# Performance work log

Hardware: AMD Instinct MI355X
Metric: run time of the kernel (lower is better)

Reference implementation:

```python
import jax, jax.numpy as jnp
import numpy as np

# ---- problem constants (mirror AdjustInstanceArea __init__ args) ----
NUM_NODES = 2_000_000
NUM_MOVABLE = 1_500_000
NUM_FILLER = 400_000
NUM_NETS = 1_500_000
PINS_PER_NET = 4                       # uniform netpin_start = arange(0, P+1, 4)
NUM_PINS = NUM_NETS * PINS_PER_NET
XL, XH, YL, YH = 0.0, 1000.0, 0.0, 1000.0
NBX = NBY = 512
BIN_W = (XH - XL) / NBX
BIN_H = (YH - YL) / NBY
UNIT_H_CAP = 1.5                       # unit horizontal routing capacity
UNIT_V_CAP = 1.5                       # unit vertical routing capacity
MAX_RATE = 2.0                         # max_route_opt_adjust_rate
MIN_RATE = 1.0 / MAX_RATE
EPS = 1e-6


def setup_inputs() -> dict:
    key = jax.random.key(0)
    k = jax.random.split(key, 4)
    x = jax.random.uniform(k[0], (NUM_NODES,), jnp.float32, XL, XH - 4.0)
    y = jax.random.uniform(k[1], (NUM_NODES,), jnp.float32, YL, YH - 4.0)
    pos = jnp.concatenate([x, y])                      # [2*num_nodes], x then y

    # pins clustered around net centers (realistic small net bboxes)
    rng = np.random.default_rng(0)
    centers = rng.uniform(0.0, 1000.0, size=(NUM_NETS, 1, 2)).astype(np.float32)
    jit = rng.uniform(-20.0, 20.0, size=(NUM_NETS, PINS_PER_NET, 2)).astype(np.float32)
    ppos = np.clip(centers + jit, 0.0, 1000.0)         # [nets, pins_per_net, 2], in net order

    # flat_netpin: pin ids grouped by net; pin_pos indexed by pin id
    flat_netpin = rng.permutation(NUM_PINS).astype(np.int32)
    px = np.empty(NUM_PINS, np.float32); py = np.empty(NUM_PINS, np.float32)
    px[flat_netpin] = ppos[..., 0].reshape(-1)
    py[flat_netpin] = ppos[..., 1].reshape(-1)
    pin_pos = jnp.concatenate([jnp.asarray(px), jnp.asarray(py)])  # [2*num_pins]

    pin2net = jnp.asarray(np.repeat(np.arange(NUM_NETS, dtype=np.int32), PINS_PER_NET))

    node_size_x = jax.random.uniform(k[2], (NUM_NODES,), jnp.float32, 1.0, 4.0)
    node_size_y = jax.random.uniform(k[3], (NUM_NODES,), jnp.float32, 1.0, 4.0)
    return {"pos": pos, "pin_pos": pin_pos,
            "node_size_x": node_size_x, "node_size_y": node_size_y,
            "flat_netpin": jnp.asarray(flat_netpin), "pin2net": pin2net}


def _rect_accum(vals, blx, bly, bhx, bhy):
    """Accumulate vals over inclusive bin rectangles via difference map + 2D cumsum."""
    D = jnp.zeros((NBX + 1, NBY + 1), vals.dtype)
    D = D.at[blx, bly].add(vals)
    D = D.at[bhx + 1, bly].add(-vals)
    D = D.at[blx, bhy + 1].add(-vals)
    D = D.at[bhx + 1, bhy + 1].add(vals)
    return jnp.cumsum(jnp.cumsum(D, axis=0), axis=1)[:NBX, :NBY]


def reference(pos, pin_pos, node_size_x, node_size_y, flat_netpin, pin2net):
    # ---- InstanceRouteOptimizationArea: RUDY routing demand per bin ----
    px = pin_pos[:NUM_PINS][flat_netpin].reshape(NUM_NETS, PINS_PER_NET)
    py = pin_pos[NUM_PINS:][flat_netpin].reshape(NUM_NETS, PINS_PER_NET)
    net_xl = jnp.min(px, axis=1); net_xh = jnp.max(px, axis=1)
    net_yl = jnp.min(py, axis=1); net_yh = jnp.max(py, axis=1)
    bw = net_xh - net_xl
    bh = net_yh - net_yl
    barea = jnp.maximum(bw * bh, EPS)
    dens_h = bw / barea                                # horizontal wire density
    dens_v = bh / barea                                # vertical wire density

    blx = jnp.clip(jnp.floor((net_xl - XL) / BIN_W), 0, NBX - 1).astype(jnp.int32)
    bhx = jnp.clip(jnp.floor((net_xh - XL) / BIN_W), 0, NBX - 1).astype(jnp.int32)
    bly = jnp.clip(jnp.floor((net_yl - YL) / BIN_H), 0, NBY - 1).astype(jnp.int32)
    bhy = jnp.clip(jnp.floor((net_yh - YL) / BIN_H), 0, NBY - 1).astype(jnp.int32)

    util_h = _rect_accum(dens_h, blx, bly, bhx, bhy) / UNIT_H_CAP
    util_v = _rect_accum(dens_v, blx, bly, bhx, bhy) / UNIT_V_CAP

    # per-movable-node utilization (gather at node center bin)
    x = pos[:NUM_NODES]; y = pos[NUM_NODES:]
    nsx_m = node_size_x[:NUM_MOVABLE]; nsy_m = node_size_y[:NUM_MOVABLE]
    cx = x[:NUM_MOVABLE] + 0.5 * nsx_m
    cy = y[:NUM_MOVABLE] + 0.5 * nsy_m
    bix = jnp.clip(jnp.floor((cx - XL) / BIN_W), 0, NBX - 1).astype(jnp.int32)
    biy = jnp.clip(jnp.floor((cy - YL) / BIN_H), 0, NBY - 1).astype(jnp.int32)
    util = jnp.maximum(util_h[bix, biy], util_v[bix, biy])
    ratio = jnp.clip(util, MIN_RATE, MAX_RATE)

    area_old = nsx_m * nsy_m
    instance_route_area = area_old * ratio

    # ---- AdjustInstanceArea: rescale under max_total_area budget ----
    filler_area_old = jnp.sum(node_size_x[NUM_NODES - NUM_FILLER:] *
                              node_size_y[NUM_NODES - NUM_FILLER:])
    max_total_area = jnp.sum(area_old) + filler_area_old
    scale = jnp.minimum(1.0, max_total_area / jnp.maximum(jnp.sum(instance_route_area), EPS))
    new_area = instance_route_area * scale
    sr = jnp.sqrt(new_area / jnp.maximum(area_old, EPS))
    nsx_new = nsx_m * sr
    nsy_new = nsy_m * sr

    # keep cell centers fixed while resizing
    x_out = x.at[:NUM_MOVABLE].add(0.5 * (nsx_m - nsx_new))
    y_out = y.at[:NUM_MOVABLE].add(0.5 * (nsy_m - nsy_new))

    # fillers absorb leftover area budget
    fscale = jnp.sqrt(jnp.maximum(max_total_area - jnp.sum(new_area), 0.0) /
                      jnp.maximum(filler_area_old, EPS))
    nsx_out = node_size_x.at[:NUM_MOVABLE].set(nsx_new)
    nsx_out = nsx_out.at[NUM_NODES - NUM_FILLER:].multiply(fscale)
    nsy_out = node_size_y.at[:NUM_MOVABLE].set(nsy_new)
    nsy_out = nsy_out.at[NUM_NODES - NUM_FILLER:].multiply(fscale)

    return jnp.concatenate([x_out, y_out, nsx_out, nsy_out])  # [4*num_nodes]
```

## Files before the change

### kernel.cpp

```cpp
#include <hip/hip_runtime.h>
#include <math.h>

#define N_NODES   2000000
#define N_MOVABLE 1500000
#define N_FILLER  400000
#define N_NETS    1500000
#define N_PINS    (N_NETS * 4)
#define NB        512
#define NT        16
#define TILE      32
#define NBUCKET   (NT * NT)
#define CAP       10240
#define NMAPS     8
#define RED_BLOCKS 512
#define NPB       2048

__device__ __forceinline__ int bin_idx(float v) {
    float b = floorf(v / 1.953125f);
    b = fminf(fmaxf(b, 0.0f), 511.0f);
    return (int)b;
}

__global__ void pack_kernel(const float* __restrict__ pin_pos,
                            float2* __restrict__ pp) {
    int i = blockIdx.x * blockDim.x + threadIdx.x;
    if (i >= N_PINS / 4) return;
    float4 a = reinterpret_cast<const float4*>(pin_pos)[i];
    float4 b = reinterpret_cast<const float4*>(pin_pos + N_PINS)[i];
    float4* o = reinterpret_cast<float4*>(pp + 4 * (size_t)i);
    o[0] = make_float4(a.x, b.x, a.y, b.y);
    o[1] = make_float4(a.z, b.z, a.w, b.w);
}

template <bool PACKED>
__device__ __forceinline__ float4 make_rec(const float* __restrict__ pin_pos,
                                           const float2* __restrict__ pp,
                                           int4 fp, int* bucket) {
    float2 p0, p1, p2, p3;
    if (PACKED) {
        p0 = pp[fp.x]; p1 = pp[fp.y]; p2 = pp[fp.z]; p3 = pp[fp.w];
    } else {
        p0 = make_float2(pin_pos[fp.x], pin_pos[N_PINS + fp.x]);
        p1 = make_float2(pin_pos[fp.y], pin_pos[N_PINS + fp.y]);
        p2 = make_float2(pin_pos[fp.z], pin_pos[N_PINS + fp.z]);
        p3 = make_float2(pin_pos[fp.w], pin_pos[N_PINS + fp.w]);
    }
    float xl = fminf(fminf(p0.x, p1.x), fminf(p2.x, p3.x));
    float xh = fmaxf(fmaxf(p0.x, p1.x), fmaxf(p2.x, p3.x));
    float yl = fminf(fminf(p0.y, p1.y), fminf(p2.y, p3.y));
    float yh = fmaxf(fmaxf(p0.y, p1.y), fmaxf(p2.y, p3.y));
    float bw = xh - xl, bh = yh - yl;
    float barea = fmaxf(bw * bh, 1e-6f);
    float vh = (bw / barea) * (1.0f / 1.5f);
    float vv = (bh / barea) * (1.0f / 1.5f);
    unsigned blx = bin_idx(xl), bhx = bin_idx(xh);
    unsigned bly = bin_idx(yl), bhy = bin_idx(yh);
    *bucket = (int)((bly >> 5) * NT + (blx >> 5));
    float4 r;
    r.x = vh; r.y = vv;
    r.z = __uint_as_float(blx | (bly << 16));
    r.w = __uint_as_float((bhx + 1) | ((bhy + 1) << 16));
    return r;
}

template <bool PACKED>
__global__ __launch_bounds__(1024)
void gather_bin_kernel(const float* __restrict__ pin_pos,
                       const float2* __restrict__ pp,
                       const int*  __restrict__ fnp,
                       float4* __restrict__ slab,
                       unsigned* __restrict__ g_ptr) {
    __shared__ unsigned hist[NBUCKET];
    __shared__ unsigned base[NBUCKET];
    int t = threadIdx.x;
    if (t < NBUCKET) hist[t] = 0;
    __syncthreads();

    int n0 = blockIdx.x * NPB + t;
    int n1 = n0 + 1024;
    bool v0 = (n0 < N_NETS), v1 = (n1 < N_NETS);

    int4 fpA = v0 ? *reinterpret_cast<const int4*>(fnp + 4 * (size_t)n0) : make_int4(0,0,0,0);
    int4 fpB = v1 ? *reinterpret_cast<const int4*>(fnp + 4 * (size_t)n1) : make_int4(0,0,0,0);

    float4 r0, r1; int b0 = 0, b1 = 0; unsigned rk0 = 0, rk1 = 0;
    if (v0) { r0 = make_rec<PACKED>(pin_pos, pp, fpA, &b0); rk0 = atomicAdd(&hist[b0], 1u); }
    if (v1) { r1 = make_rec<PACKED>(pin_pos, pp, fpB, &b1); rk1 = atomicAdd(&hist[b1], 1u); }
    __syncthreads();
    if (t < NBUCKET) {
        unsigned c = hist[t];
        base[t] = c ? atomicAdd(&g_ptr[t], c) : 0u;
    }
    __syncthreads();
    if (v0) { unsigned s = base[b0] + rk0; if (s < CAP) slab[(size_t)b0 * CAP + s] = r0; }
    if (v1) { unsigned s = base[b1] + rk1; if (s < CAP) slab[(size_t)b1 * CAP + s] = r1; }
}

__global__ __launch_bounds__(256)
void accum_kernel(const float4* __restrict__ slab,
                  const unsigned* __restrict__ g_cnt,
                  float2* __restrict__ Dp) {
    __shared__ float2 acc[64 * 64];
    int wg = blockIdx.x;
    int h = wg & 1, tile = wg >> 1;
    int tx = tile & (NT - 1), ty = tile >> 4;

    for (int i = threadIdx.x; i < 64 * 64; i += 256) acc[i] = make_float2(0.f, 0.f);
    __syncthreads();

    int x0 = tx * TILE, y0 = ty * TILE;
    unsigned cnt = min(g_cnt[tile], (unsigned)CAP);
    unsigned lo = h ? cnt / 2 : 0u;
    unsigned hi = h ? cnt : cnt / 2;
    const float4* recs = slab + (size_t)tile * CAP;

    for (unsigned i = lo + threadIdx.x; i < hi; i += 256) {
        float4 r = recs[i];
        unsigned zlo = __float_as_uint(r.z), zhi = __float_as_uint(r.w);
        int ax0 = (int)(zlo & 0xffffu), ay0 = (int)(zlo >> 16);
        int ax1 = (int)(zhi & 0xffffu), ay1 = (int)(zhi >> 16);
        int X0 = ax0 - x0, Y0 = ay0 - y0;
        int X1 = ax1 - x0, Y1 = ay1 - y0;
        bool okx1 = (ax1 < NB), oky1 = (ay1 < NB);
        atomicAdd(&acc[X0 * 64 + Y0].x,  r.x);
        atomicAdd(&acc[X0 * 64 + Y0].y,  r.y);
        if (okx1) { atomicAdd(&acc[X1 * 64 + Y0].x, -r.x); atomicAdd(&acc[X1 * 64 + Y0].y, -r.y); }
        if (oky1) { atomicAdd(&acc[X0 * 64 + Y1].x, -r.x); atomicAdd(&acc[X0 * 64 + Y1].y, -r.y); }
        if (okx1 && oky1) { atomicAdd(&acc[X1 * 64 + Y1].x, r.x); atomicAdd(&acc[X1 * 64 + Y1].y, r.y); }
    }
    __syncthreads();

    int m = h * 4 + (ty & 1) * 2 + (tx & 1);
    float2* D = Dp + (size_t)m * NB * NB;
    for (int i = threadIdx.x; i < 64 * 64; i += 256) {
        int X = i >> 6, Y = i & 63;
        int gx = x0 + X, gy = y0 + Y;
        if (gx < NB && gy < NB) D[(size_t)gx * NB + gy] = acc[i];
    }
}

__global__ void scanA_kernel(const float2* __restrict__ Dp,
                             float2* __restrict__ S) {
    __shared__ float2 s[NB];
    int x = blockIdx.x, t = threadIdx.x;
    float2 a = make_float2(0.f, 0.f);
    #pragma unroll
    for (int m = 0; m < NMAPS; ++m) {
        if (((m & 1) && x < TILE) || ((m & 2) && t < TILE)) continue;
        float2 v = Dp[(size_t)m * NB * NB + (size_t)x * NB + t];
        a.x += v.x; a.y += v.y;
    }
    s[t] = a;
    __syncthreads();
    for (int off = 1; off < NB; off <<= 1) {
        float2 u = s[t];
        if (t >= off) { float2 w = s[t - off]; u.x += w.x; u.y += w.y; }
        __syncthreads();
        s[t] = u;
        __syncthreads();
    }
    S[(size_t)x * NB + t] = s[t];
}

__global__ void scanB_kernel(float2* __restrict__ S) {
    __shared__ float2 s[NB];
    int y = blockIdx.x, t = threadIdx.x;
    s[t] = S[(size_t)t * NB + y];
    __syncthreads();
    for (int off = 1; off < NB; off <<= 1) {
        float2 u = s[t];
        if (t >= off) { float2 w = s[t - off]; u.x += w.x; u.y += w.y; }
        __syncthreads();
        s[t] = u;
        __syncthreads();
    }
    S[(size_t)t * NB + y] = s[t];
}

__global__ __launch_bounds__(256)
void reduce_kernel(const float* __restrict__ pos,
                   const float* __restrict__ nsx,
                   const float* __restrict__ nsy,
                   const float2* __restrict__ S,
                   double* __restrict__ partials) {
    const int MQ = N_MOVABLE / 4;
    const int TQ = MQ + N_FILLER / 4;
    double a_old = 0.0, a_route = 0.0, a_fill = 0.0;
    int stride = gridDim.x * blockDim.x;
    for (int q = blockIdx.x * blockDim.x + threadIdx.x; q < TQ; q += stride) {
        if (q < MQ) {
            int i = 4 * q;
            float4 x4  = *reinterpret_cast<const float4*>(pos + i);
            float4 y4  = *reinterpret_cast<const float4*>(pos + N_NODES + i);
            float4 sx4 = *reinterpret_cast<const float4*>(nsx + i);
            float4 sy4 = *reinterpret_cast<const float4*>(nsy + i);
            float xs[4] = {x4.x, x4.y, x4.z, x4.w};
            float ys[4] = {y4.x, y4.y, y4.z, y4.w};
            float sxs[4] = {sx4.x, sx4.y, sx4.z, sx4.w};
            float sys[4] = {sy4.x, sy4.y, sy4.z, sy4.w};
            #pragma unroll
            for (int k = 0; k < 4; ++k) {
                int bx = bin_idx(xs[k] + 0.5f * sxs[k]);
                int by = bin_idx(ys[k] + 0.5f * sys[k]);
                float2 u2 = S[(size_t)bx * NB + by];
                float ratio = fminf(fmaxf(fmaxf(u2.x, u2.y), 0.5f), 2.0f);
                float area = sxs[k] * sys[k];
                a_old += (double)area;
                a_route += (double)(area * ratio);
            }
        } else {
            int j = (N_NODES - N_FILLER) + 4 * (q - MQ);
            float4 sx4 = *reinterpret_cast<const float4*>(nsx + j);
            float4 sy4 = *reinterpret_cast<const float4*>(nsy + j);
            a_fill += (double)(sx4.x * sy4.x + sx4.y * sy4.y +
                               sx4.z * sy4.z + sx4.w * sy4.w);
        }
    }
    for (int off = 32; off > 0; off >>= 1) {
        a_old   += __shfl_down(a_old, off);
        a_route += __shfl_down(a_route, off);
        a_fill  += __shfl_down(a_fill, off);
    }
    __shared__ double sd[4][3];
    int wid = threadIdx.x >> 6, lane = threadIdx.x & 63;
    if (lane == 0) { sd[wid][0] = a_old; sd[wid][1] = a_route; sd[wid][2] = a_fill; }
    __syncthreads();
    if (threadIdx.x == 0) {
        double s0 = 0, s1 = 0, s2 = 0;
        for (int w = 0; w < 4; ++w) { s0 += sd[w][0]; s1 += sd[w][1]; s2 += sd[w][2]; }
        partials[blockIdx.x * 3 + 0] = s0;
        partials[blockIdx.x * 3 + 1] = s1;
        partials[blockIdx.x * 3 + 2] = s2;
    }
}

__global__ void finish_kernel(const double* __restrict__ partials,
                              double* __restrict__ sums) {
    int t = threadIdx.x;
    double s0 = partials[t * 3 + 0];
    double s1 = partials[t * 3 + 1];
    double s2 = partials[t * 3 + 2];
    for (int off = 32; off > 0; off >>= 1) {
        s0 += __shfl_down(s0, off);
        s1 += __shfl_down(s1, off);
        s2 += __shfl_down(s2, off);
    }
    __shared__ double sd[8][3];
    int wid = t >> 6, lane = t & 63;
    if (lane == 0) { sd[wid][0] = s0; sd[wid][1] = s1; sd[wid][2] = s2; }
    __syncthreads();
    if (t == 0) {
        double a = 0, b = 0, c = 0;
        for (int w = 0; w < 8; ++w) { a += sd[w][0]; b += sd[w][1]; c += sd[w][2]; }
        sums[0] = a; sums[1] = b; sums[2] = c;
    }
}

__global__ __launch_bounds__(256)
void final_kernel(const float* __restrict__ pos,
                  const float* __restrict__ nsx,
                  const float* __restrict__ nsy,
                  const float2* __restrict__ S,
                  const double* __restrict__ sums,
                  float* __restrict__ out) {
    double sum_area  = sums[0];
    double sum_route = sums[1];
    double fill_old  = sums[2];
    double max_total = sum_area + fill_old;

    float scale = fminf(1.0f, (float)(max_total / fmax(sum_route, 1e-6)));
    float sum_new = (float)(scale * (float)sum_route);
    float fscale = sqrtf(fmaxf((float)max_total - sum_new, 0.0f) /
                         fmaxf((float)fill_old, 1e-6f));

    int q = blockIdx.x * blockDim.x + threadIdx.x;
    if (q >= N_NODES / 4) return;
    int i = 4 * q;

    float4 x4  = *reinterpret_cast<const float4*>(pos + i);
    float4 y4  = *reinterpret_cast<const float4*>(pos + N_NODES + i);
    float4 sx4 = *reinterpret_cast<const float4*>(nsx + i);
    float4 sy4 = *reinterpret_cast<const float4*>(nsy + i);

    float xs[4] = {x4.x, x4.y, x4.z, x4.w};
    float ys[4] = {y4.x, y4.y, y4.z, y4.w};
    float sxs[4] = {sx4.x, sx4.y, sx4.z, sx4.w};
    float sys[4] = {sy4.x, sy4.y, sy4.z, sy4.w};

    if (i < N_MOVABLE) {
        #pragma unroll
        for (int k = 0; k < 4; ++k) {
            int bx = bin_idx(xs[k] + 0.5f * sxs[k]);
            int by = bin_idx(ys[k] + 0.5f * sys[k]);
            float2 u2 = S[(size_t)bx * NB + by];
            float ratio = fminf(fmaxf(fmaxf(u2.x, u2.y), 0.5f), 2.0f);
            float area = sxs[k] * sys[k];
            float new_area = area * ratio * scale;
            float sr = sqrtf(new_area / fmaxf(area, 1e-6f));
            float sx_new = sxs[k] * sr, sy_new = sys[k] * sr;
            xs[k] = xs[k] + 0.5f * (sxs[k] - sx_new);
            ys[k] = ys[k] + 0.5f * (sys[k] - sy_new);
            sxs[k] = sx_new; sys[k] = sy_new;
        }
    } else if (i >= N_NODES - N_FILLER) {
        #pragma unroll
        for (int k = 0; k < 4; ++k) { sxs[k] *= fscale; sys[k] *= fscale; }
    }

    *reinterpret_cast<float4*>(out + i)               = make_float4(xs[0], xs[1], xs[2], xs[3]);
    *reinterpret_cast<float4*>(out + N_NODES + i)     = make_float4(ys[0], ys[1], ys[2], ys[3]);
    *reinterpret_cast<float4*>(out + 2 * N_NODES + i) = make_float4(sxs[0], sxs[1], sxs[2], sxs[3]);
    *reinterpret_cast<float4*>(out + 3 * N_NODES + i) = make_float4(sys[0], sys[1], sys[2], sys[3]);
}

extern "C" void kernel_launch(void* const* d_in, const int* in_sizes, int n_in,
                              void* d_out, int out_size, void* d_ws, size_t ws_size,
                              hipStream_t stream) {
    const float* pos         = (const float*)d_in[0];
    const float* pin_pos     = (const float*)d_in[1];
    const float* nsx         = (const float*)d_in[2];
    const float* nsy         = (const float*)d_in[3];
    const int*   flat_netpin = (const int*)d_in[4];
    float* out = (float*)d_out;

    const size_t pp_b   = (size_t)N_PINS * sizeof(float2);
    const size_t slab_b = (size_t)NBUCKET * CAP * sizeof(float4);
    const size_t dp_b   = (size_t)NMAPS * NB * NB * sizeof(float2);
    const size_t s_b    = (size_t)NB * NB * sizeof(float2);
    const size_t part_b = (size_t)RED_BLOCKS * 3 * sizeof(double);
    const size_t gp_b   = 4096;

    const size_t need_primary = pp_b + slab_b + gp_b + 64;

    float2* pp = nullptr;
    float4* slab; float2* Dp; float2* S; double* partials;
    unsigned* g_ptr; double* sums;
    char* base = (char*)d_ws;
    bool packed = (ws_size >= need_primary);
    if (packed) {
        pp       = (float2*)base;
        Dp       = (float2*)base;
        S        = (float2*)(base + dp_b);
        partials = (double*)(base + dp_b + s_b);
        slab     = (float4*)(base + pp_b);
        g_ptr    = (unsigned*)(base + pp_b + slab_b);
        sums     = (double*)(base + pp_b + slab_b + gp_b);
    } else {
        slab     = (float4*)base;
        Dp       = (float2*)(base + slab_b);
        S        = (float2*)(base + slab_b + dp_b);
        partials = (double*)(base + slab_b + dp_b + s_b);
        g_ptr    = (unsigned*)(base + slab_b + dp_b + s_b + part_b);
        sums     = (double*)((char*)g_ptr + gp_b);
    }

    hipMemsetAsync(g_ptr, 0, NBUCKET * sizeof(unsigned), stream);

    const int GB_BLOCKS = (N_NETS + NPB - 1) / NPB;
    if (packed) {
        pack_kernel<<<(N_PINS / 4 + 255) / 256, 256, 0, stream>>>(pin_pos, pp);
        gather_bin_kernel<true><<<GB_BLOCKS, 1024, 0, stream>>>(pin_pos, pp, flat_netpin, slab, g_ptr);
    } else {
        gather_bin_kernel<false><<<GB_BLOCKS, 1024, 0, stream>>>(pin_pos, nullptr, flat_netpin, slab, g_ptr);
    }

    accum_kernel<<<2 * NBUCKET, 256, 0, stream>>>(slab, g_ptr, Dp);
    scanA_kernel<<<NB, NB, 0, stream>>>(Dp, S);
    scanB_kernel<<<NB, NB, 0, stream>>>(S);

    reduce_kernel<<<RED_BLOCKS, 256, 0, stream>>>(pos, nsx, nsy, S, partials);
    finish_kernel<<<1, 512, 0, stream>>>(partials, sums);
    final_kernel<<<(N_NODES / 4 + 255) / 256, 256, 0, stream>>>(pos, nsx, nsy, S, sums, out);
}
```

Before: 267.9 us.

## Fuse post-binning stages into one cooperative persistent kernel with grid syncs

Replaces the accum, two scan, reduce, finish and final launches with one cooperative mega-kernel of 1024 blocks that separates the stages with grid-wide syncs, and keeps the separate launches as a fallback. Accumulation is split four ways per tile (16 partial maps), gather handles four nets per thread, scans use 256 threads with two elements each, and the g_ptr memset moves into pack_kernel. The goal is to remove launch gaps and tail effects between small stages. In exchange it adds grid-sync cost, requires co-residency of 1024 blocks with 32KB LDS each, and doubles the size of the partial-map buffer.

Result: slower. 797.5 us (+197.7%).

```diff
diff --git a/kernel.cpp b/kernel.cpp
--- a/kernel.cpp
+++ b/kernel.cpp
@@ -1,4 +1,5 @@
 #include <hip/hip_runtime.h>
+#include <hip/hip_cooperative_groups.h>
 #include <math.h>
 
 #define N_NODES   2000000
@@ -11,9 +12,12 @@
 #define TILE      32
 #define NBUCKET   (NT * NT)
 #define CAP       10240
-#define NMAPS     8
-#define RED_BLOCKS 512
-#define NPB       2048
+#define NMAPS     16
+#define NPB       4096
+#define MEGA_BLOCKS 1024
+#define GSZ       (MEGA_BLOCKS * 256)
+
+namespace cg = cooperative_groups;
 
 __device__ __forceinline__ int bin_idx(float v) {
     float b = floorf(v / 1.953125f);
@@ -22,7 +26,9 @@
 }
 
 __global__ void pack_kernel(const float* __restrict__ pin_pos,
-                            float2* __restrict__ pp) {
+                            float2* __restrict__ pp,
+                            unsigned* __restrict__ g_ptr) {
+    if (blockIdx.x == 0 && threadIdx.x < NBUCKET) g_ptr[threadIdx.x] = 0u;
     int i = blockIdx.x * blockDim.x + threadIdx.x;
     if (i >= N_PINS / 4) return;
     float4 a = reinterpret_cast<const float4*>(pin_pos)[i];
@@ -77,44 +83,56 @@
     __syncthreads();
 
     int n0 = blockIdx.x * NPB + t;
-    int n1 = n0 + 1024;
-    bool v0 = (n0 < N_NETS), v1 = (n1 < N_NETS);
-
-    int4 fpA = v0 ? *reinterpret_cast<const int4*>(fnp + 4 * (size_t)n0) : make_int4(0,0,0,0);
-    int4 fpB = v1 ? *reinterpret_cast<const int4*>(fnp + 4 * (size_t)n1) : make_int4(0,0,0,0);
-
-    float4 r0, r1; int b0 = 0, b1 = 0; unsigned rk0 = 0, rk1 = 0;
-    if (v0) { r0 = make_rec<PACKED>(pin_pos, pp, fpA, &b0); rk0 = atomicAdd(&hist[b0], 1u); }
-    if (v1) { r1 = make_rec<PACKED>(pin_pos, pp, fpB, &b1); rk1 = atomicAdd(&hist[b1], 1u); }
+    bool v[4]; int4 fp[4]; float4 r[4]; int b[4]; unsigned rk[4];
+    #pragma unroll
+    for (int k = 0; k < 4; ++k) {
+        int n = n0 + k * 1024;
+        v[k] = (n < N_NETS);
+        fp[k] = v[k] ? *reinterpret_cast<const int4*>(fnp + 4 * (size_t)n)
+                     : make_int4(0, 0, 0, 0);
+    }
+    #pragma unroll
+    for (int k = 0; k < 4; ++k) {
+        b[k] = 0;
+        if (v[k]) r[k] = make_rec<PACKED>(pin_pos, pp, fp[k], &b[k]);
+    }
+    #pragma unroll
+    for (int k = 0; k < 4; ++k) {
+        rk[k] = v[k] ? atomicAdd(&hist[b[k]], 1u) : 0u;
+    }
     __syncthreads();
     if (t < NBUCKET) {
         unsigned c = hist[t];
         base[t] = c ? atomicAdd(&g_ptr[t], c) : 0u;
     }
     __syncthreads();
-    if (v0) { unsigned s = base[b0] + rk0; if (s < CAP) slab[(size_t)b0 * CAP + s] = r0; }
-    if (v1) { unsigned s = base[b1] + rk1; if (s < CAP) slab[(size_t)b1 * CAP + s] = r1; }
-}
-
-__global__ __launch_bounds__(256)
-void accum_kernel(const float4* __restrict__ slab,
-                  const unsigned* __restrict__ g_cnt,
-                  float2* __restrict__ Dp) {
-    __shared__ float2 acc[64 * 64];
-    int wg = blockIdx.x;
-    int h = wg & 1, tile = wg >> 1;
+    #pragma unroll
+    for (int k = 0; k < 4; ++k) {
+        if (v[k]) {
+            unsigned s = base[b[k]] + rk[k];
+            if (s < CAP) slab[(size_t)b[k] * CAP + s] = r[k];
+        }
+    }
+}
+
+
+__device__ __forceinline__ void stage_accum(const float4* __restrict__ slab,
+                                            const unsigned* __restrict__ g_cnt,
+                                            float2* __restrict__ Dp,
+                                            float2* acc, int wg, int tid) {
+    int h = wg & 3, tile = wg >> 2;
     int tx = tile & (NT - 1), ty = tile >> 4;
 
-    for (int i = threadIdx.x; i < 64 * 64; i += 256) acc[i] = make_float2(0.f, 0.f);
+    for (int i = tid; i < 64 * 64; i += 256) acc[i] = make_float2(0.f, 0.f);
     __syncthreads();
 
     int x0 = tx * TILE, y0 = ty * TILE;
     unsigned cnt = min(g_cnt[tile], (unsigned)CAP);
-    unsigned lo = h ? cnt / 2 : 0u;
-    unsigned hi = h ? cnt : cnt / 2;
+    unsigned lo = (cnt * (unsigned)h) >> 2;
+    unsigned hi = (cnt * (unsigned)(h + 1)) >> 2;
     const float4* recs = slab + (size_t)tile * CAP;
 
-    for (unsigned i = lo + threadIdx.x; i < hi; i += 256) {
+    for (unsigned i = lo + tid; i < hi; i += 256) {
         float4 r = recs[i];
         unsigned zlo = __float_as_uint(r.z), zhi = __float_as_uint(r.w);
         int ax0 = (int)(zlo & 0xffffu), ay0 = (int)(zlo >> 16);
@@ -132,62 +150,72 @@
 
     int m = h * 4 + (ty & 1) * 2 + (tx & 1);
     float2* D = Dp + (size_t)m * NB * NB;
-    for (int i = threadIdx.x; i < 64 * 64; i += 256) {
+    for (int i = tid; i < 64 * 64; i += 256) {
         int X = i >> 6, Y = i & 63;
         int gx = x0 + X, gy = y0 + Y;
         if (gx < NB && gy < NB) D[(size_t)gx * NB + gy] = acc[i];
     }
 }
 
-__global__ void scanA_kernel(const float2* __restrict__ Dp,
-                             float2* __restrict__ S) {
-    __shared__ float2 s[NB];
-    int x = blockIdx.x, t = threadIdx.x;
-    float2 a = make_float2(0.f, 0.f);
+__device__ __forceinline__ void stage_scanA(const float2* __restrict__ Dp,
+                                            float2* __restrict__ S,
+                                            float2* s, int x, int tid) {
     #pragma unroll
-    for (int m = 0; m < NMAPS; ++m) {
-        if (((m & 1) && x < TILE) || ((m & 2) && t < TILE)) continue;
-        float2 v = Dp[(size_t)m * NB * NB + (size_t)x * NB + t];
-        a.x += v.x; a.y += v.y;
-    }
-    s[t] = a;
+    for (int k = 0; k < 2; ++k) {
+        int y = tid + k * 256;
+        float2 a = make_float2(0.f, 0.f);
+        #pragma unroll
+        for (int m = 0; m < NMAPS; ++m) {
+            if (((m & 1) && x < TILE) || ((m & 2) && y < TILE)) continue;
+            float2 v = Dp[(size_t)m * NB * NB + (size_t)x * NB + y];
+            a.x += v.x; a.y += v.y;
+        }
+        s[y] = a;
+    }
     __syncthreads();
     for (int off = 1; off < NB; off <<= 1) {
-        float2 u = s[t];
-        if (t >= off) { float2 w = s[t - off]; u.x += w.x; u.y += w.y; }
+        float2 u0 = s[tid], u1 = s[tid + 256];
+        float2 w0 = (tid >= off) ? s[tid - off] : make_float2(0.f, 0.f);
+        float2 w1 = s[tid + 256 - off];
         __syncthreads();
-        s[t] = u;
+        if (tid >= off) { u0.x += w0.x; u0.y += w0.y; }
+        u1.x += w1.x; u1.y += w1.y;
+        s[tid] = u0; s[tid + 256] = u1;
         __syncthreads();
     }
-    S[(size_t)x * NB + t] = s[t];
-}
-
-__global__ void scanB_kernel(float2* __restrict__ S) {
-    __shared__ float2 s[NB];
-    int y = blockIdx.x, t = threadIdx.x;
-    s[t] = S[(size_t)t * NB + y];
+    S[(size_t)x * NB + tid] = s[tid];
+    S[(size_t)x * NB + tid + 256] = s[tid + 256];
+}
+
+__device__ __forceinline__ void stage_scanB(float2* __restrict__ S,
+                                            float2* s, int y, int tid) {
+    s[tid] = S[(size_t)tid * NB + y];
+    s[tid + 256] = S[(size_t)(tid + 256) * NB + y];
     __syncthreads();
     for (int off = 1; off < NB; off <<= 1) {
-        float2 u = s[t];
-        if (t >= off) { float2 w = s[t - off]; u.x += w.x; u.y += w.y; }
+        float2 u0 = s[tid], u1 = s[tid + 256];
+        float2 w0 = (tid >= off) ? s[tid - off] : make_float2(0.f, 0.f);
+        float2 w1 = s[tid + 256 - off];
         __syncthreads();
-        s[t] = u;
+        if (tid >= off) { u0.x += w0.x; u0.y += w0.y; }
+        u1.x += w1.x; u1.y += w1.y;
+        s[tid] = u0; s[tid + 256] = u1;
         __syncthreads();
     }
-    S[(size_t)t * NB + y] = s[t];
-}
-
-__global__ __launch_bounds__(256)
-void reduce_kernel(const float* __restrict__ pos,
-                   const float* __restrict__ nsx,
-                   const float* __restrict__ nsy,
-                   const float2* __restrict__ S,
-                   double* __restrict__ partials) {
+    S[(size_t)tid * NB + y] = s[tid];
+    S[(size_t)(tid + 256) * NB + y] = s[tid + 256];
+}
+
+__device__ __forceinline__ void stage_reduce(const float* __restrict__ pos,
+                                             const float* __restrict__ nsx,
+                                             const float* __restrict__ nsy,
+                                             const float2* __restrict__ S,
+                                             double* __restrict__ partials,
+                                             float2* smem, int bid, int tid) {
     const int MQ = N_MOVABLE / 4;
     const int TQ = MQ + N_FILLER / 4;
     double a_old = 0.0, a_route = 0.0, a_fill = 0.0;
-    int stride = gridDim.x * blockDim.x;
-    for (int q = blockIdx.x * blockDim.x + threadIdx.x; q < TQ; q += stride) {
+    for (int q = bid * 256 + tid; q < TQ; q += GSZ) {
         if (q < MQ) {
             int i = 4 * q;
             float4 x4  = *reinterpret_cast<const float4*>(pos + i);
@@ -221,96 +249,159 @@
         a_route += __shfl_down(a_route, off);
         a_fill  += __shfl_down(a_fill, off);
     }
-    __shared__ double sd[4][3];
-    int wid = threadIdx.x >> 6, lane = threadIdx.x & 63;
-    if (lane == 0) { sd[wid][0] = a_old; sd[wid][1] = a_route; sd[wid][2] = a_fill; }
-    __syncthreads();
-    if (threadIdx.x == 0) {
+    double* sd = (double*)smem;
+    int wid = tid >> 6, lane = tid & 63;
+    if (lane == 0) { sd[wid * 3 + 0] = a_old; sd[wid * 3 + 1] = a_route; sd[wid * 3 + 2] = a_fill; }
+    __syncthreads();
+    if (tid == 0) {
         double s0 = 0, s1 = 0, s2 = 0;
-        for (int w = 0; w < 4; ++w) { s0 += sd[w][0]; s1 += sd[w][1]; s2 += sd[w][2]; }
-        partials[blockIdx.x * 3 + 0] = s0;
-        partials[blockIdx.x * 3 + 1] = s1;
-        partials[blockIdx.x * 3 + 2] = s2;
-    }
-}
-
-__global__ void finish_kernel(const double* __restrict__ partials,
-                              double* __restrict__ sums) {
-    int t = threadIdx.x;
-    double s0 = partials[t * 3 + 0];
-    double s1 = partials[t * 3 + 1];
-    double s2 = partials[t * 3 + 2];
+        for (int w = 0; w < 4; ++w) { s0 += sd[w * 3]; s1 += sd[w * 3 + 1]; s2 += sd[w * 3 + 2]; }
+        partials[bid * 3 + 0] = s0;
+        partials[bid * 3 + 1] = s1;
+        partials[bid * 3 + 2] = s2;
+    }
+}
+
+__device__ __forceinline__ void stage_finish(const double* __restrict__ partials,
+                                             double* __restrict__ sums,
+                                             float2* smem, int tid) {
+    double s0 = 0, s1 = 0, s2 = 0;
+    for (int r = tid; r < MEGA_BLOCKS; r += 256) {
+        s0 += partials[r * 3 + 0];
+        s1 += partials[r * 3 + 1];
+        s2 += partials[r * 3 + 2];
+    }
     for (int off = 32; off > 0; off >>= 1) {
         s0 += __shfl_down(s0, off);
         s1 += __shfl_down(s1, off);
         s2 += __shfl_down(s2, off);
     }
-    __shared__ double sd[8][3];
-    int wid = t >> 6, lane = t & 63;
-    if (lane == 0) { sd[wid][0] = s0; sd[wid][1] = s1; sd[wid][2] = s2; }
-    __syncthreads();
-    if (t == 0) {
+    double* sd = (double*)smem;
+    int wid = tid >> 6, lane = tid & 63;
+    if (lane == 0) { sd[wid * 3 + 0] = s0; sd[wid * 3 + 1] = s1; sd[wid * 3 + 2] = s2; }
+    __syncthreads();
+    if (tid == 0) {
         double a = 0, b = 0, c = 0;
-        for (int w = 0; w < 8; ++w) { a += sd[w][0]; b += sd[w][1]; c += sd[w][2]; }
+        for (int w = 0; w < 4; ++w) { a += sd[w * 3]; b += sd[w * 3 + 1]; c += sd[w * 3 + 2]; }
         sums[0] = a; sums[1] = b; sums[2] = c;
     }
 }
 
-__global__ __launch_bounds__(256)
-void final_kernel(const float* __restrict__ pos,
-                  const float* __restrict__ nsx,
-                  const float* __restrict__ nsy,
-                  const float2* __restrict__ S,
-                  const double* __restrict__ sums,
-                  float* __restrict__ out) {
+__device__ __forceinline__ void stage_final(const float* __restrict__ pos,
+                                            const float* __restrict__ nsx,
+                                            const float* __restrict__ nsy,
+                                            const float2* __restrict__ S,
+                                            const double* __restrict__ sums,
+                                            float* __restrict__ out,
+                                            int bid, int tid) {
     double sum_area  = sums[0];
     double sum_route = sums[1];
     double fill_old  = sums[2];
     double max_total = sum_area + fill_old;
-
     float scale = fminf(1.0f, (float)(max_total / fmax(sum_route, 1e-6)));
     float sum_new = (float)(scale * (float)sum_route);
     float fscale = sqrtf(fmaxf((float)max_total - sum_new, 0.0f) /
                          fmaxf((float)fill_old, 1e-6f));
 
-    int q = blockIdx.x * blockDim.x + threadIdx.x;
-    if (q >= N_NODES / 4) return;
-    int i = 4 * q;
-
-    float4 x4  = *reinterpret_cast<const float4*>(pos + i);
-    float4 y4  = *reinterpret_cast<const float4*>(pos + N_NODES + i);
-    float4 sx4 = *reinterpret_cast<const float4*>(nsx + i);
-    float4 sy4 = *reinterpret_cast<const float4*>(nsy + i);
-
-    float xs[4] = {x4.x, x4.y, x4.z, x4.w};
-    float ys[4] = {y4.x, y4.y, y4.z, y4.w};
-    float sxs[4] = {sx4.x, sx4.y, sx4.z, sx4.w};
-    float sys[4] = {sy4.x, sy4.y, sy4.z, sy4.w};
-
-    if (i < N_MOVABLE) {
-        #pragma unroll
-        for (int k = 0; k < 4; ++k) {
-            int bx = bin_idx(xs[k] + 0.5f * sxs[k]);
-            int by = bin_idx(ys[k] + 0.5f * sys[k]);
-            float2 u2 = S[(size_t)bx * NB + by];
-            float ratio = fminf(fmaxf(fmaxf(u2.x, u2.y), 0.5f), 2.0f);
-            float area = sxs[k] * sys[k];
-            float new_area = area * ratio * scale;
-            float sr = sqrtf(new_area / fmaxf(area, 1e-6f));
-            float sx_new = sxs[k] * sr, sy_new = sys[k] * sr;
-            xs[k] = xs[k] + 0.5f * (sxs[k] - sx_new);
-            ys[k] = ys[k] + 0.5f * (sys[k] - sy_new);
-            sxs[k] = sx_new; sys[k] = sy_new;
+    for (int q = bid * 256 + tid; q < N_NODES / 4; q += GSZ) {
+        int i = 4 * q;
+        float4 x4  = *reinterpret_cast<const float4*>(pos + i);
+        float4 y4  = *reinterpret_cast<const float4*>(pos + N_NODES + i);
+        float4 sx4 = *reinterpret_cast<const float4*>(nsx + i);
+        float4 sy4 = *reinterpret_cast<const float4*>(nsy + i);
+        float xs[4] = {x4.x, x4.y, x4.z, x4.w};
+        float ys[4] = {y4.x, y4.y, y4.z, y4.w};
+        float sxs[4] = {sx4.x, sx4.y, sx4.z, sx4.w};
+        float sys[4] = {sy4.x, sy4.y, sy4.z, sy4.w};
+
+        if (i < N_MOVABLE) {
+            #pragma unroll
+            for (int k = 0; k < 4; ++k) {
+                int bx = bin_idx(xs[k] + 0.5f * sxs[k]);
+                int by = bin_idx(ys[k] + 0.5f * sys[k]);
+                float2 u2 = S[(size_t)bx * NB + by];
+                float ratio = fminf(fmaxf(fmaxf(u2.x, u2.y), 0.5f), 2.0f);
+                float area = sxs[k] * sys[k];
+                float new_area = area * ratio * scale;
+                float sr = sqrtf(new_area / fmaxf(area, 1e-6f));
+                float sx_new = sxs[k] * sr, sy_new = sys[k] * sr;
+                xs[k] = xs[k] + 0.5f * (sxs[k] - sx_new);
+                ys[k] = ys[k] + 0.5f * (sys[k] - sy_new);
+                sxs[k] = sx_new; sys[k] = sy_new;
+            }
+        } else if (i >= N_NODES - N_FILLER) {
+            #pragma unroll
+            for (int k = 0; k < 4; ++k) { sxs[k] *= fscale; sys[k] *= fscale; }
         }
-    } else if (i >= N_NODES - N_FILLER) {
-        #pragma unroll
-        for (int k = 0; k < 4; ++k) { sxs[k] *= fscale; sys[k] *= fscale; }
-    }
-
-    *reinterpret_cast<float4*>(out + i)               = make_float4(xs[0], xs[1], xs[2], xs[3]);
-    *reinterpret_cast<float4*>(out + N_NODES + i)     = make_float4(ys[0], ys[1], ys[2], ys[3]);
-    *reinterpret_cast<float4*>(out + 2 * N_NODES + i) = make_float4(sxs[0], sxs[1], sxs[2], sxs[3]);
-    *reinterpret_cast<float4*>(out + 3 * N_NODES + i) = make_float4(sys[0], sys[1], sys[2], sys[3]);
+
+        *reinterpret_cast<float4*>(out + i)               = make_float4(xs[0], xs[1], xs[2], xs[3]);
+        *reinterpret_cast<float4*>(out + N_NODES + i)     = make_float4(ys[0], ys[1], ys[2], ys[3]);
+        *reinterpret_cast<float4*>(out + 2 * N_NODES + i) = make_float4(sxs[0], sxs[1], sxs[2], sxs[3]);
+        *reinterpret_cast<float4*>(out + 3 * N_NODES + i) = make_float4(sys[0], sys[1], sys[2], sys[3]);
+    }
+}
+
+__global__ __launch_bounds__(256)
+void mega_kernel(const float4* __restrict__ slab,
+                 const unsigned* __restrict__ g_cnt,
+                 float2* __restrict__ Dp,
+                 float2* __restrict__ S,
+                 const float* __restrict__ pos,
+                 const float* __restrict__ nsx,
+                 const float* __restrict__ nsy,
+                 double* __restrict__ partials,
+                 double* __restrict__ sums,
+                 float* __restrict__ out) {
+    __shared__ float2 smem[4096];
+    cg::grid_group g = cg::this_grid();
+    int bid = blockIdx.x, tid = threadIdx.x;
+
+    stage_accum(slab, g_cnt, Dp, smem, bid, tid);
+    g.sync();
+    if (bid < NB) stage_scanA(Dp, S, smem, bid, tid);
+    g.sync();
+    if (bid < NB) stage_scanB(S, smem, bid, tid);
+    g.sync();
+    stage_reduce(pos, nsx, nsy, S, partials, smem, bid, tid);
+    g.sync();
+    if (bid == 0) stage_finish(partials, sums, smem, tid);
+    g.sync();
+    stage_final(pos, nsx, nsy, S, sums, out, bid, tid);
+}
+
+__global__ __launch_bounds__(256)
+void accum_kernel(const float4* __restrict__ slab, const unsigned* __restrict__ g_cnt,
+                  float2* __restrict__ Dp) {
+    __shared__ float2 smem[4096];
+    stage_accum(slab, g_cnt, Dp, smem, blockIdx.x, threadIdx.x);
+}
+__global__ __launch_bounds__(256)
+void scanA_kernel(const float2* __restrict__ Dp, float2* __restrict__ S) {
+    __shared__ float2 s[NB];
+    stage_scanA(Dp, S, s, blockIdx.x, threadIdx.x);
+}
+__global__ __launch_bounds__(256)
+void scanB_kernel(float2* __restrict__ S) {
+    __shared__ float2 s[NB];
+    stage_scanB(S, s, blockIdx.x, threadIdx.x);
+}
+__global__ __launch_bounds__(256)
+void reduce_kernel(const float* __restrict__ pos, const float* __restrict__ nsx,
+                   const float* __restrict__ nsy, const float2* __restrict__ S,
+                   double* __restrict__ partials) {
+    __shared__ float2 smem[64];
+    stage_reduce(pos, nsx, nsy, S, partials, smem, blockIdx.x, threadIdx.x);
+}
+__global__ __launch_bounds__(256)
+void finish_kernel(const double* __restrict__ partials, double* __restrict__ sums) {
+    __shared__ float2 smem[64];
+    stage_finish(partials, sums, smem, threadIdx.x);
+}
+__global__ __launch_bounds__(256)
+void final_kernel(const float* __restrict__ pos, const float* __restrict__ nsx,
+                  const float* __restrict__ nsy, const float2* __restrict__ S,
+                  const double* __restrict__ sums, float* __restrict__ out) {
+    stage_final(pos, nsx, nsy, S, sums, out, blockIdx.x, threadIdx.x);
 }
 
 extern "C" void kernel_launch(void* const* d_in, const int* in_sizes, int n_in,
@@ -327,48 +418,60 @@
     const size_t slab_b = (size_t)NBUCKET * CAP * sizeof(float4);
     const size_t dp_b   = (size_t)NMAPS * NB * NB * sizeof(float2);
     const size_t s_b    = (size_t)NB * NB * sizeof(float2);
-    const size_t part_b = (size_t)RED_BLOCKS * 3 * sizeof(double);
+    const size_t part_b = (size_t)MEGA_BLOCKS * 3 * sizeof(double);
     const size_t gp_b   = 4096;
 
-    const size_t need_primary = pp_b + slab_b + gp_b + 64;
-
-    float2* pp = nullptr;
-    float4* slab; float2* Dp; float2* S; double* partials;
-    unsigned* g_ptr; double* sums;
+    const size_t need_primary = pp_b + slab_b + gp_b + 256;
+
     char* base = (char*)d_ws;
     bool packed = (ws_size >= need_primary);
+
+    float2* pp; float4* slab; float2* Dp; float2* S;
+    double* partials; double* sums; unsigned* g_ptr;
     if (packed) {
         pp       = (float2*)base;
         Dp       = (float2*)base;
         S        = (float2*)(base + dp_b);
         partials = (double*)(base + dp_b + s_b);
+        sums     = (double*)(base + dp_b + s_b + part_b);
         slab     = (float4*)(base + pp_b);
         g_ptr    = (unsigned*)(base + pp_b + slab_b);
-        sums     = (double*)(base + pp_b + slab_b + gp_b);
     } else {
+        pp       = nullptr;
         slab     = (float4*)base;
         Dp       = (float2*)(base + slab_b);
         S        = (float2*)(base + slab_b + dp_b);
         partials = (double*)(base + slab_b + dp_b + s_b);
-        g_ptr    = (unsigned*)(base + slab_b + dp_b + s_b + part_b);
-        sums     = (double*)((char*)g_ptr + gp_b);
-    }
-
-    hipMemsetAsync(g_ptr, 0, NBUCKET * sizeof(unsigned), stream);
+        sums     = (double*)(base + slab_b + dp_b + s_b + part_b);
+        g_ptr    = (unsigned*)(base + slab_b + dp_b + s_b + part_b + 64);
+    }
 
     const int GB_BLOCKS = (N_NETS + NPB - 1) / NPB;
     if (packed) {
-        pack_kernel<<<(N_PINS / 4 + 255) / 256, 256, 0, stream>>>(pin_pos, pp);
+        pack_kernel<<<(N_PINS / 4 + 255) / 256, 256, 0, stream>>>(pin_pos, pp, g_ptr);
         gather_bin_kernel<true><<<GB_BLOCKS, 1024, 0, stream>>>(pin_pos, pp, flat_netpin, slab, g_ptr);
     } else {
+        hipMemsetAsync(g_ptr, 0, NBUCKET * sizeof(unsigned), stream);
         gather_bin_kernel<false><<<GB_BLOCKS, 1024, 0, stream>>>(pin_pos, nullptr, flat_netpin, slab, g_ptr);
     }
 
-    accum_kernel<<<2 * NBUCKET, 256, 0, stream>>>(slab, g_ptr, Dp);
-    scanA_kernel<<<NB, NB, 0, stream>>>(Dp, S);
-    scanB_kernel<<<NB, NB, 0, stream>>>(S);
-
-    reduce_kernel<<<RED_BLOCKS, 256, 0, stream>>>(pos, nsx, nsy, S, partials);
-    finish_kernel<<<1, 512, 0, stream>>>(partials, sums);
-    final_kernel<<<(N_NODES / 4 + 255) / 256, 256, 0, stream>>>(pos, nsx, nsy, S, sums, out);
-}
+    const float4* slab_c = slab;
+    const unsigned* gc = g_ptr;
+    const float* pos_c = pos; const float* nsx_c = nsx; const float* nsy_c = nsy;
+    float* out_l = out;
+    void* args[] = { (void*)&slab_c, (void*)&gc, (void*)&Dp, (void*)&S,
+                     (void*)&pos_c, (void*)&nsx_c, (void*)&nsy_c,
+                     (void*)&partials, (void*)&sums, (void*)&out_l };
+    hipError_t e = hipLaunchCooperativeKernel((void*)mega_kernel,
+                                              dim3(MEGA_BLOCKS), dim3(256),
+                                              args, 0, stream);
+    if (e != hipSuccess) {
+        (void)hipGetLastError();
+        accum_kernel <<<MEGA_BLOCKS, 256, 0, stream>>>(slab, g_ptr, Dp);
+        scanA_kernel <<<NB, 256, 0, stream>>>(Dp, S);
+        scanB_kernel <<<NB, 256, 0, stream>>>(S);
+        reduce_kernel<<<MEGA_BLOCKS, 256, 0, stream>>>(pos, nsx, nsy, S, partials);
+        finish_kernel<<<1, 256, 0, stream>>>(partials, sums);
+        final_kernel <<<MEGA_BLOCKS, 256, 0, stream>>>(pos, nsx, nsy, S, sums, out);
+    }
+}
```

## Switch accumulation to owner-tile gather with 4 slices, fewer maps, fused memset

Applied to the files above, without the earlier changes.

The accumulation kernel now has each 32x32 output tile pull records from its own bucket and the left, up and up-left neighbor buckets, split into four slices. It writes only its own tile instead of a 64x64 overlapping halo into parity-indexed maps, so the D maps drop from 8 to 4 and scanA stops skipping per-parity regions. The gather kernel processes 4 nets per thread, the g_ptr memset is folded into pack_kernel, and the reduce block count doubles with a strided finish loop. The aim is less shared memory per block, fewer global map writes and reads, and one less launch. The cost is that each accum block now reads up to four buckets' records and filters out most of them.

Result: faster. 242.1 us (-9.6%).

```diff
diff --git a/kernel.cpp b/kernel.cpp
--- a/kernel.cpp
+++ b/kernel.cpp
@@ -11,9 +11,10 @@
 #define TILE      32
 #define NBUCKET   (NT * NT)
 #define CAP       10240
-#define NMAPS     8
-#define RED_BLOCKS 512
-#define NPB       2048
+#define NSLICE    4
+#define NMAPS     NSLICE
+#define NPB       4096
+#define RED_BLOCKS 1024
 
 __device__ __forceinline__ int bin_idx(float v) {
     float b = floorf(v / 1.953125f);
@@ -22,7 +23,9 @@
 }
 
 __global__ void pack_kernel(const float* __restrict__ pin_pos,
-                            float2* __restrict__ pp) {
+                            float2* __restrict__ pp,
+                            unsigned* __restrict__ g_ptr) {
+    if (blockIdx.x == 0 && threadIdx.x < NBUCKET) g_ptr[threadIdx.x] = 0u;
     int i = blockIdx.x * blockDim.x + threadIdx.x;
     if (i >= N_PINS / 4) return;
     float4 a = reinterpret_cast<const float4*>(pin_pos)[i];
@@ -77,76 +80,108 @@
     __syncthreads();
 
     int n0 = blockIdx.x * NPB + t;
-    int n1 = n0 + 1024;
-    bool v0 = (n0 < N_NETS), v1 = (n1 < N_NETS);
-
-    int4 fpA = v0 ? *reinterpret_cast<const int4*>(fnp + 4 * (size_t)n0) : make_int4(0,0,0,0);
-    int4 fpB = v1 ? *reinterpret_cast<const int4*>(fnp + 4 * (size_t)n1) : make_int4(0,0,0,0);
-
-    float4 r0, r1; int b0 = 0, b1 = 0; unsigned rk0 = 0, rk1 = 0;
-    if (v0) { r0 = make_rec<PACKED>(pin_pos, pp, fpA, &b0); rk0 = atomicAdd(&hist[b0], 1u); }
-    if (v1) { r1 = make_rec<PACKED>(pin_pos, pp, fpB, &b1); rk1 = atomicAdd(&hist[b1], 1u); }
+    bool v[4]; int4 fp[4]; float4 r[4]; int b[4]; unsigned rk[4];
+    #pragma unroll
+    for (int k = 0; k < 4; ++k) {
+        int n = n0 + k * 1024;
+        v[k] = (n < N_NETS);
+        fp[k] = v[k] ? *reinterpret_cast<const int4*>(fnp + 4 * (size_t)n)
+                     : make_int4(0, 0, 0, 0);
+    }
+    #pragma unroll
+    for (int k = 0; k < 4; ++k) {
+        b[k] = 0;
+        if (v[k]) r[k] = make_rec<PACKED>(pin_pos, pp, fp[k], &b[k]);
+    }
+    #pragma unroll
+    for (int k = 0; k < 4; ++k) {
+        rk[k] = v[k] ? atomicAdd(&hist[b[k]], 1u) : 0u;
+    }
     __syncthreads();
     if (t < NBUCKET) {
         unsigned c = hist[t];
         base[t] = c ? atomicAdd(&g_ptr[t], c) : 0u;
     }
     __syncthreads();
-    if (v0) { unsigned s = base[b0] + rk0; if (s < CAP) slab[(size_t)b0 * CAP + s] = r0; }
-    if (v1) { unsigned s = base[b1] + rk1; if (s < CAP) slab[(size_t)b1 * CAP + s] = r1; }
+    #pragma unroll
+    for (int k = 0; k < 4; ++k) {
+        if (v[k]) {
+            unsigned s = base[b[k]] + rk[k];
+            if (s < CAP) slab[(size_t)b[k] * CAP + s] = r[k];
+        }
+    }
+}
+
+__device__ __forceinline__ void rec_process(float4 r, int x0, int y0,
+                                            float2* acc) {
+    unsigned zlo = __float_as_uint(r.z), zhi = __float_as_uint(r.w);
+    int ax0 = (int)(zlo & 0xffffu), ay0 = (int)(zlo >> 16);
+    int ax1 = (int)(zhi & 0xffffu), ay1 = (int)(zhi >> 16);
+    int X0 = ax0 - x0, Y0 = ay0 - y0;
+    int X1 = ax1 - x0, Y1 = ay1 - y0;
+    bool iX0 = (unsigned)X0 < TILE, iX1 = (unsigned)X1 < TILE;
+    bool iY0 = (unsigned)Y0 < TILE, iY1 = (unsigned)Y1 < TILE;
+    if (iX0 && iY0) { atomicAdd(&acc[X0 * TILE + Y0].x,  r.x); atomicAdd(&acc[X0 * TILE + Y0].y,  r.y); }
+    if (iX1 && iY0) { atomicAdd(&acc[X1 * TILE + Y0].x, -r.x); atomicAdd(&acc[X1 * TILE + Y0].y, -r.y); }
+    if (iX0 && iY1) { atomicAdd(&acc[X0 * TILE + Y1].x, -r.x); atomicAdd(&acc[X0 * TILE + Y1].y, -r.y); }
+    if (iX1 && iY1) { atomicAdd(&acc[X1 * TILE + Y1].x,  r.x); atomicAdd(&acc[X1 * TILE + Y1].y,  r.y); }
 }
 
 __global__ __launch_bounds__(256)
 void accum_kernel(const float4* __restrict__ slab,
                   const unsigned* __restrict__ g_cnt,
                   float2* __restrict__ Dp) {
-    __shared__ float2 acc[64 * 64];
+    __shared__ float2 acc[TILE * TILE];
     int wg = blockIdx.x;
-    int h = wg & 1, tile = wg >> 1;
+    int sl = wg & (NSLICE - 1), tile = wg >> 2;
     int tx = tile & (NT - 1), ty = tile >> 4;
-
-    for (int i = threadIdx.x; i < 64 * 64; i += 256) acc[i] = make_float2(0.f, 0.f);
+    int tid = threadIdx.x;
+
+    for (int i = tid; i < TILE * TILE; i += 256) acc[i] = make_float2(0.f, 0.f);
     __syncthreads();
 
     int x0 = tx * TILE, y0 = ty * TILE;
-    unsigned cnt = min(g_cnt[tile], (unsigned)CAP);
-    unsigned lo = h ? cnt / 2 : 0u;
-    unsigned hi = h ? cnt : cnt / 2;
-    const float4* recs = slab + (size_t)tile * CAP;
-
-    for (unsigned i = lo + threadIdx.x; i < hi; i += 256) {
-        float4 r = recs[i];
-        unsigned zlo = __float_as_uint(r.z), zhi = __float_as_uint(r.w);
-        int ax0 = (int)(zlo & 0xffffu), ay0 = (int)(zlo >> 16);
-        int ax1 = (int)(zhi & 0xffffu), ay1 = (int)(zhi >> 16);
-        int X0 = ax0 - x0, Y0 = ay0 - y0;
-        int X1 = ax1 - x0, Y1 = ay1 - y0;
-        bool okx1 = (ax1 < NB), oky1 = (ay1 < NB);
-        atomicAdd(&acc[X0 * 64 + Y0].x,  r.x);
-        atomicAdd(&acc[X0 * 64 + Y0].y,  r.y);
-        if (okx1) { atomicAdd(&acc[X1 * 64 + Y0].x, -r.x); atomicAdd(&acc[X1 * 64 + Y0].y, -r.y); }
-        if (oky1) { atomicAdd(&acc[X0 * 64 + Y1].x, -r.x); atomicAdd(&acc[X0 * 64 + Y1].y, -r.y); }
-        if (okx1 && oky1) { atomicAdd(&acc[X1 * 64 + Y1].x, r.x); atomicAdd(&acc[X1 * 64 + Y1].y, r.y); }
-    }
-    __syncthreads();
-
-    int m = h * 4 + (ty & 1) * 2 + (tx & 1);
-    float2* D = Dp + (size_t)m * NB * NB;
-    for (int i = threadIdx.x; i < 64 * 64; i += 256) {
-        int X = i >> 6, Y = i & 63;
-        int gx = x0 + X, gy = y0 + Y;
-        if (gx < NB && gy < NB) D[(size_t)gx * NB + gy] = acc[i];
-    }
-}
-
-__global__ void scanA_kernel(const float2* __restrict__ Dp,
-                             float2* __restrict__ S) {
+    #pragma unroll
+    for (int dy = -1; dy <= 0; ++dy) {
+        int sy = ty + dy; if (sy < 0) continue;
+        #pragma unroll
+        for (int dx = -1; dx <= 0; ++dx) {
+            int sx = tx + dx; if (sx < 0) continue;
+            int sb = sy * NT + sx;
+            unsigned cnt = min(g_cnt[sb], (unsigned)CAP);
+            unsigned lo = (cnt * (unsigned)sl) >> 2;
+            unsigned hi = (cnt * (unsigned)(sl + 1)) >> 2;
+            const float4* recs = slab + (size_t)sb * CAP;
+            unsigned i = lo + tid;
+            for (; i + 768 < hi; i += 1024) {
+                float4 r0 = recs[i];
+                float4 r1 = recs[i + 256];
+                float4 r2 = recs[i + 512];
+                float4 r3 = recs[i + 768];
+                rec_process(r0, x0, y0, acc);
+                rec_process(r1, x0, y0, acc);
+                rec_process(r2, x0, y0, acc);
+                rec_process(r3, x0, y0, acc);
+            }
+            for (; i < hi; i += 256) rec_process(recs[i], x0, y0, acc);
+        }
+    }
+    __syncthreads();
+
+    float2* D = Dp + (size_t)sl * NB * NB;
+    for (int i = tid; i < TILE * TILE; i += 256) {
+        int X = i >> 5, Y = i & 31;
+        D[(size_t)(x0 + X) * NB + (y0 + Y)] = acc[i];
+    }
+}
+
+__global__ __launch_bounds__(512)
+void scanA_kernel(const float2* __restrict__ Dp, float2* __restrict__ S) {
     __shared__ float2 s[NB];
     int x = blockIdx.x, t = threadIdx.x;
     float2 a = make_float2(0.f, 0.f);
     #pragma unroll
     for (int m = 0; m < NMAPS; ++m) {
-        if (((m & 1) && x < TILE) || ((m & 2) && t < TILE)) continue;
         float2 v = Dp[(size_t)m * NB * NB + (size_t)x * NB + t];
         a.x += v.x; a.y += v.y;
     }
@@ -162,7 +197,8 @@
     S[(size_t)x * NB + t] = s[t];
 }
 
-__global__ void scanB_kernel(float2* __restrict__ S) {
+__global__ __launch_bounds__(512)
+void scanB_kernel(float2* __restrict__ S) {
     __shared__ float2 s[NB];
     int y = blockIdx.x, t = threadIdx.x;
     s[t] = S[(size_t)t * NB + y];
@@ -234,24 +270,28 @@
     }
 }
 
-__global__ void finish_kernel(const double* __restrict__ partials,
-                              double* __restrict__ sums) {
+__global__ __launch_bounds__(256)
+void finish_kernel(const double* __restrict__ partials,
+                   double* __restrict__ sums) {
     int t = threadIdx.x;
-    double s0 = partials[t * 3 + 0];
-    double s1 = partials[t * 3 + 1];
-    double s2 = partials[t * 3 + 2];
+    double s0 = 0, s1 = 0, s2 = 0;
+    for (int r = t; r < RED_BLOCKS; r += 256) {
+        s0 += partials[r * 3 + 0];
+        s1 += partials[r * 3 + 1];
+        s2 += partials[r * 3 + 2];
+    }
     for (int off = 32; off > 0; off >>= 1) {
         s0 += __shfl_down(s0, off);
         s1 += __shfl_down(s1, off);
         s2 += __shfl_down(s2, off);
     }
-    __shared__ double sd[8][3];
+    __shared__ double sd[4][3];
     int wid = t >> 6, lane = t & 63;
     if (lane == 0) { sd[wid][0] = s0; sd[wid][1] = s1; sd[wid][2] = s2; }
     __syncthreads();
     if (t == 0) {
         double a = 0, b = 0, c = 0;
-        for (int w = 0; w < 8; ++w) { a += sd[w][0]; b += sd[w][1]; c += sd[w][2]; }
+        for (int w = 0; w < 4; ++w) { a += sd[w][0]; b += sd[w][1]; c += sd[w][2]; }
         sums[0] = a; sums[1] = b; sums[2] = c;
     }
 }
@@ -330,45 +370,44 @@
     const size_t part_b = (size_t)RED_BLOCKS * 3 * sizeof(double);
     const size_t gp_b   = 4096;
 
-    const size_t need_primary = pp_b + slab_b + gp_b + 64;
-
-    float2* pp = nullptr;
-    float4* slab; float2* Dp; float2* S; double* partials;
-    unsigned* g_ptr; double* sums;
+    const size_t need_primary = pp_b + slab_b + gp_b + 256;
+
     char* base = (char*)d_ws;
     bool packed = (ws_size >= need_primary);
+
+    float2* pp; float4* slab; float2* Dp; float2* S;
+    double* partials; double* sums; unsigned* g_ptr;
     if (packed) {
         pp       = (float2*)base;
         Dp       = (float2*)base;
         S        = (float2*)(base + dp_b);
         partials = (double*)(base + dp_b + s_b);
+        sums     = (double*)(base + dp_b + s_b + part_b);
         slab     = (float4*)(base + pp_b);
         g_ptr    = (unsigned*)(base + pp_b + slab_b);
-        sums     = (double*)(base + pp_b + slab_b + gp_b);
     } else {
+        pp       = nullptr;
         slab     = (float4*)base;
         Dp       = (float2*)(base + slab_b);
         S        = (float2*)(base + slab_b + dp_b);
         partials = (double*)(base + slab_b + dp_b + s_b);
-        g_ptr    = (unsigned*)(base + slab_b + dp_b + s_b + part_b);
-        sums     = (double*)((char*)g_ptr + gp_b);
-    }
-
-    hipMemsetAsync(g_ptr, 0, NBUCKET * sizeof(unsigned), stream);
+        sums     = (double*)(base + slab_b + dp_b + s_b + part_b);
+        g_ptr    = (unsigned*)(base + slab_b + dp_b + s_b + part_b + 64);
+    }
 
     const int GB_BLOCKS = (N_NETS + NPB - 1) / NPB;
     if (packed) {
-        pack_kernel<<<(N_PINS / 4 + 255) / 256, 256, 0, stream>>>(pin_pos, pp);
+        pack_kernel<<<(N_PINS / 4 + 255) / 256, 256, 0, stream>>>(pin_pos, pp, g_ptr);
         gather_bin_kernel<true><<<GB_BLOCKS, 1024, 0, stream>>>(pin_pos, pp, flat_netpin, slab, g_ptr);
     } else {
+        hipMemsetAsync(g_ptr, 0, NBUCKET * sizeof(unsigned), stream);
         gather_bin_kernel<false><<<GB_BLOCKS, 1024, 0, stream>>>(pin_pos, nullptr, flat_netpin, slab, g_ptr);
     }
 
-    accum_kernel<<<2 * NBUCKET, 256, 0, stream>>>(slab, g_ptr, Dp);
-    scanA_kernel<<<NB, NB, 0, stream>>>(Dp, S);
-    scanB_kernel<<<NB, NB, 0, stream>>>(S);
-
+    accum_kernel <<<NBUCKET * NSLICE, 256, 0, stream>>>(slab, g_ptr, Dp);
+    scanA_kernel <<<NB, 512, 0, stream>>>(Dp, S);
+    scanB_kernel <<<NB, 512, 0, stream>>>(S);
     reduce_kernel<<<RED_BLOCKS, 256, 0, stream>>>(pos, nsx, nsy, S, partials);
-    finish_kernel<<<1, 512, 0, stream>>>(partials, sums);
-    final_kernel<<<(N_NODES / 4 + 255) / 256, 256, 0, stream>>>(pos, nsx, nsy, S, sums, out);
-}
+    finish_kernel<<<1, 256, 0, stream>>>(partials, sums);
+    final_kernel <<<(N_NODES / 4 + 255) / 256, 256, 0, stream>>>(pos, nsx, nsy, S, sums, out);
+}
```
